# Kernel tuning notes

Measured on AMD Instinct MI355X. Metric: run time of the kernel, lower is better.

The kernel has to match this reference:

```python
import jax, jax.numpy as jnp
import numpy as np

N, G, D, H, F, L, NH_CI = 4096, 1024, 128, 4, 512, 2, 2
HD = D // H
LBD = 1.0
LS = 100.0  # length_scale, non-trainable


def setup_inputs() -> dict:
    key = jax.random.key(0)
    ks = jax.random.split(key, 40)
    s = 0.05
    r = lambda i, shape: (jax.random.normal(ks[i], shape, jnp.float32) * s)
    inp = {
        'raw_expr': jax.random.normal(ks[0], (N, G), jnp.float32),
        'sqr_pdist': jax.random.uniform(ks[1], (N, N), jnp.float32) * 1e4,
        'dn_W1': r(2, (G, 512)), 'dn_b1': jnp.zeros((512,), jnp.float32),
        'dn_W2': r(3, (512, G)), 'dn_b2': jnp.zeros((G,), jnp.float32),
        'q_W1': r(4, (G, 64)), 'q_b1': jnp.zeros((64,), jnp.float32),
        'q_W2': r(5, (64, 1)), 'q_b2': jnp.zeros((1,), jnp.float32),
        'e_Win': r(6, (G, D)), 'e_bin': jnp.zeros((D,), jnp.float32),
        'Wq': r(7, (L, D, D)), 'Wk': r(8, (L, D, D)),
        'Wv': r(9, (L, D, D)), 'Wo': r(10, (L, D, D)),
        'bq': jnp.zeros((L, D), jnp.float32), 'bk': jnp.zeros((L, D), jnp.float32),
        'bv': jnp.zeros((L, D), jnp.float32), 'bo': jnp.zeros((L, D), jnp.float32),
        'ln1_g': jnp.ones((L, D), jnp.float32), 'ln1_b': jnp.zeros((L, D), jnp.float32),
        'ln2_g': jnp.ones((L, D), jnp.float32), 'ln2_b': jnp.zeros((L, D), jnp.float32),
        'f_W1': r(11, (L, D, F)), 'f_b1': jnp.zeros((L, F), jnp.float32),
        'f_W2': r(12, (L, F, D)), 'f_b2': jnp.zeros((L, D), jnp.float32),
        'ci_T': r(13, (NH_CI, D, D)), 'ci_G': r(14, (NH_CI, G, G)),
        'interact': 1,
    }
    return inp


def _ln(x, g, b):
    m = jnp.mean(x, -1, keepdims=True)
    v = jnp.var(x, -1, keepdims=True)
    return g * (x - m) / jnp.sqrt(v + 1e-5) + b


def _forward(raw_expr, sqr_pdist, dn_W1, dn_b1, dn_W2, dn_b2,
             q_W1, q_b1, q_W2, q_b2, e_Win, e_bin,
             Wq, Wk, Wv, Wo, bq, bk, bv, bo,
             ln1_g, ln1_b, ln2_g, ln2_b, f_W1, f_b1, f_W2, f_b2,
             ci_T, ci_G, interact):
    n_cells = raw_expr.shape[0]
    # CellDenoise: residual MLP
    denoised = jax.nn.relu(raw_expr @ dn_W1 + dn_b1) @ dn_W2 + dn_b2 + raw_expr
    # CellQualify: [N, 1]
    quality = jnp.tanh(raw_expr @ q_W1 + q_b1) @ q_W2 + q_b2
    # CellEmbed: input proj + transformer encoder blocks over cells (no batch)
    h = raw_expr @ e_Win + e_bin  # [N, D]
    for l in range(L):
        q = (h @ Wq[l] + bq[l]).reshape(n_cells, H, HD)
        k = (h @ Wk[l] + bk[l]).reshape(n_cells, H, HD)
        v = (h @ Wv[l] + bv[l]).reshape(n_cells, H, HD)
        scores = jnp.einsum('nhd,mhd->hnm', q, k) / jnp.sqrt(jnp.float32(HD))
        attn = jax.nn.softmax(scores, axis=-1)
        o = jnp.einsum('hnm,mhd->nhd', attn, v).reshape(n_cells, D) @ Wo[l] + bo[l]
        h = _ln(h + o, ln1_g[l], ln1_b[l])
        ff = jax.nn.relu(h @ f_W1[l] + f_b1[l]) @ f_W2[l] + f_b2[l]
        h = _ln(h + ff, ln2_g[l], ln2_b[l])
    emb = h  # [N, D]
    # CellSmooth: softmax(-cdist + quality^T) @ denoised
    sq = jnp.sum(emb * emb, -1)
    d2 = jnp.maximum(sq[:, None] + sq[None, :] - 2.0 * emb @ emb.T, 0.0)
    dist = jnp.sqrt(d2)
    sim = jax.nn.softmax(-dist + quality.T, axis=-1)  # [N, N]
    smoothed = sim @ denoised  # [N, G]
    if interact:
        spatial = jnp.exp(-sqr_pdist / (LS * LS))  # [N, N]
        ci_out = jnp.zeros_like(smoothed)
        for hh in range(NH_CI):
            cell_inter = jax.nn.sigmoid(emb @ ci_T[hh] @ emb.T)  # [N, N]
            ci_out = ci_out + (spatial * cell_inter) @ smoothed @ ci_G[hh] / smoothed.shape[1]
        return smoothed + LBD * ci_out
    return smoothed


def reference(raw_expr, sqr_pdist, dn_W1, dn_b1, dn_W2, dn_b2,
              q_W1, q_b1, q_W2, q_b2, e_Win, e_bin,
              Wq, Wk, Wv, Wo, bq, bk, bv, bo,
              ln1_g, ln1_b, ln2_g, ln2_b, f_W1, f_b1, f_W2, f_b2,
              ci_T, ci_G, interact):
    return _forward(raw_expr, sqr_pdist, dn_W1, dn_b1, dn_W2, dn_b2,
                    q_W1, q_b1, q_W2, q_b2, e_Win, e_bin,
                    Wq, Wk, Wv, Wo, bq, bk, bv, bo,
                    ln1_g, ln1_b, ln2_g, ln2_b, f_W1, f_b1, f_W2, f_b2,
                    ci_T, ci_G, interact)
```

## Files before the change

### kernel.cpp

```cpp
#include <hip/hip_runtime.h>
#include <hip/hip_bf16.h>

#define NC 4096
#define GG 1024
#define DM 128
#define HH 4
#define HDIM 32
#define FF 512
#define LL 2
#define NHCI 2
#define NSF 16
#define LDV (NC+64)
#define LS2 (100.0f*100.0f)
#define QSCALE 0.17677669529663687f

typedef __bf16 bf16x8 __attribute__((ext_vector_type(8)));
typedef __bf16 bf16x4 __attribute__((ext_vector_type(4)));
typedef float  f32x4  __attribute__((ext_vector_type(4)));

__device__ __forceinline__ int xcd_swz(int orig, int nwg)
{
    int q = nwg >> 3, r = nwg & 7;
    int xcd = orig & 7, idx = orig >> 3;
    return (xcd < r ? xcd*(q+1) : r*(q+1) + (xcd-r)*q) + idx;
}

enum { MM_NONE=0, MM_BIAS, MM_BIAS_B16, MM_RELU_B16, MM_B16, MM_SIGSP_B16, MM_DIST };

template<int EM>
__launch_bounds__(256)
__global__ void mgemm_k(const __bf16* __restrict__ A, int lda,
                        const __bf16* __restrict__ BT, int ldb,
                        const float* __restrict__ aux1,
                        float* __restrict__ C, __bf16* __restrict__ Cb, int ldc,
                        int M, int N, int K, float alpha,
                        const float* __restrict__ aux2,
                        const int* __restrict__ flag)
{
    if (flag && *flag == 0) return;
    __shared__ __align__(16) __bf16 As[128][32];
    __shared__ __align__(16) __bf16 Bs[128][32];
    const int tid  = threadIdx.x;
    const int lane = tid & 63;
    const int wid  = tid >> 6;
    const int wm = wid >> 1, wn = wid & 1;
    const int nwg  = gridDim.x * gridDim.y;
    const int wg   = xcd_swz(blockIdx.y * gridDim.x + blockIdx.x, nwg);
    const int bm = (wg / gridDim.x) * 128, bn = (wg % gridDim.x) * 128;

    f32x4 acc[4][4];
    #pragma unroll
    for (int m=0;m<4;m++)
        #pragma unroll
        for (int n=0;n<4;n++) acc[m][n] = (f32x4){0.f,0.f,0.f,0.f};

    const int c0 = wid*64 + lane, c1 = c0 + 256;
    const __bf16* ga0 = A  + (size_t)(bm + (c0>>2))*lda + ((c0&3)<<3);
    const __bf16* ga1 = A  + (size_t)(bm + (c1>>2))*lda + ((c1&3)<<3);
    const __bf16* gb0 = BT + (size_t)(bn + (c0>>2))*ldb + ((c0&3)<<3);
    const __bf16* gb1 = BT + (size_t)(bn + (c1>>2))*ldb + ((c1&3)<<3);
    auto* lA = (__attribute__((address_space(3))) __bf16*)&As[0][0];
    auto* lB = (__attribute__((address_space(3))) __bf16*)&Bs[0][0];
    auto* lA0 = (__attribute__((address_space(3))) void*)(lA + (size_t)(wid*64)*8);
    auto* lA1 = (__attribute__((address_space(3))) void*)(lA + (size_t)(256 + wid*64)*8);
    auto* lB0 = (__attribute__((address_space(3))) void*)(lB + (size_t)(wid*64)*8);
    auto* lB1 = (__attribute__((address_space(3))) void*)(lB + (size_t)(256 + wid*64)*8);

    const int r  = lane & 15;
    const int kb = lane >> 4;
    const int arow = wm*64, brow = wn*64;

    for (int k0 = 0; k0 < K; k0 += 32) {
        __builtin_amdgcn_global_load_lds((const __attribute__((address_space(1))) void*)ga0, lA0, 16, 0, 0);
        __builtin_amdgcn_global_load_lds((const __attribute__((address_space(1))) void*)ga1, lA1, 16, 0, 0);
        __builtin_amdgcn_global_load_lds((const __attribute__((address_space(1))) void*)gb0, lB0, 16, 0, 0);
        __builtin_amdgcn_global_load_lds((const __attribute__((address_space(1))) void*)gb1, lB1, 16, 0, 0);
        ga0 += 32; ga1 += 32; gb0 += 32; gb1 += 32;
        __syncthreads();
        bf16x8 af[4], bfr[4];
        #pragma unroll
        for (int m=0;m<4;m++) af[m]  = *(const bf16x8*)&As[arow + m*16 + r][kb*8];
        #pragma unroll
        for (int n=0;n<4;n++) bfr[n] = *(const bf16x8*)&Bs[brow + n*16 + r][kb*8];
        #pragma unroll
        for (int m=0;m<4;m++)
            #pragma unroll
            for (int n=0;n<4;n++)
                acc[m][n] = __builtin_amdgcn_mfma_f32_16x16x32_bf16(af[m], bfr[n], acc[m][n], 0, 0, 0);
        __syncthreads();
    }

    const int crow = (lane >> 4) * 4;
    const int ccol = lane & 15;
    #pragma unroll
    for (int m=0;m<4;m++) {
        #pragma unroll
        for (int n=0;n<4;n++) {
            const int gn = bn + wn*64 + n*16 + ccol;
            #pragma unroll
            for (int q=0;q<4;q++) {
                const int gm = bm + wm*64 + m*16 + crow + q;
                float v = acc[m][n][q] * alpha;
                if (EM==MM_BIAS || EM==MM_BIAS_B16 || EM==MM_RELU_B16) v += aux1[gn];
                if (EM==MM_RELU_B16) v = fmaxf(v, 0.f);
                if (EM==MM_SIGSP_B16) {
                    v = 1.f/(1.f + __expf(-v));
                    v *= __expf(aux2[(size_t)(gm >> 1)*(size_t)N + gn] * (-1.f/LS2));
                }
                if (EM==MM_DIST) {
                    float d2 = fmaxf(aux2[gm] + aux2[gn] - 2.f*v, 0.f);
                    v = __expf(aux1[gn] - sqrtf(d2));
                }
                const size_t ci = (size_t)gm*ldc + gn;
                if (EM==MM_NONE || EM==MM_BIAS) C[ci] = v;
                else Cb[ci] = (__bf16)v;
            }
        }
    }
}

__launch_bounds__(256)
__global__ void mgemm_sk(const __bf16* __restrict__ A, int lda,
                         const __bf16* __restrict__ BT, int ldb,
                         __bf16* __restrict__ P, int M, int N, int KC,
                         const int* __restrict__ flag)
{
    if (flag && *flag == 0) return;
    __shared__ __align__(16) __bf16 As[128][32];
    __shared__ __align__(16) __bf16 Bs[128][32];
    const int tid  = threadIdx.x;
    const int lane = tid & 63;
    const int wid  = tid >> 6;
    const int wm = wid >> 1, wn = wid & 1;
    const int nwg  = gridDim.x * gridDim.y;
    const int wg   = xcd_swz(blockIdx.y * gridDim.x + blockIdx.x, nwg);
    const int bm = (wg / gridDim.x) * 128, bn = (wg % gridDim.x) * 128;
    const size_t koff = (size_t)blockIdx.z * KC;

    f32x4 acc[4][4];
    #pragma unroll
    for (int m=0;m<4;m++)
        #pragma unroll
        for (int n=0;n<4;n++) acc[m][n] = (f32x4){0.f,0.f,0.f,0.f};

    const int c0 = wid*64 + lane, c1 = c0 + 256;
    const __bf16* ga0 = A  + (size_t)(bm + (c0>>2))*lda + koff + ((c0&3)<<3);
    const __bf16* ga1 = A  + (size_t)(bm + (c1>>2))*lda + koff + ((c1&3)<<3);
    const __bf16* gb0 = BT + (size_t)(bn + (c0>>2))*ldb + koff + ((c0&3)<<3);
    const __bf16* gb1 = BT + (size_t)(bn + (c1>>2))*ldb + koff + ((c1&3)<<3);
    auto* lA = (__attribute__((address_space(3))) __bf16*)&As[0][0];
    auto* lB = (__attribute__((address_space(3))) __bf16*)&Bs[0][0];
    auto* lA0 = (__attribute__((address_space(3))) void*)(lA + (size_t)(wid*64)*8);
    auto* lA1 = (__attribute__((address_space(3))) void*)(lA + (size_t)(256 + wid*64)*8);
    auto* lB0 = (__attribute__((address_space(3))) void*)(lB + (size_t)(wid*64)*8);
    auto* lB1 = (__attribute__((address_space(3))) void*)(lB + (size_t)(256 + wid*64)*8);

    const int r  = lane & 15;
    const int kb = lane >> 4;
    const int arow = wm*64, brow = wn*64;

    for (int k0 = 0; k0 < KC; k0 += 32) {
        __builtin_amdgcn_global_load_lds((const __attribute__((address_space(1))) void*)ga0, lA0, 16, 0, 0);
        __builtin_amdgcn_global_load_lds((const __attribute__((address_space(1))) void*)ga1, lA1, 16, 0, 0);
        __builtin_amdgcn_global_load_lds((const __attribute__((address_space(1))) void*)gb0, lB0, 16, 0, 0);
        __builtin_amdgcn_global_load_lds((const __attribute__((address_space(1))) void*)gb1, lB1, 16, 0, 0);
        ga0 += 32; ga1 += 32; gb0 += 32; gb1 += 32;
        __syncthreads();
        bf16x8 af[4], bfr[4];
        #pragma unroll
        for (int m=0;m<4;m++) af[m]  = *(const bf16x8*)&As[arow + m*16 + r][kb*8];
        #pragma unroll
        for (int n=0;n<4;n++) bfr[n] = *(const bf16x8*)&Bs[brow + n*16 + r][kb*8];
        #pragma unroll
        for (int m=0;m<4;m++)
            #pragma unroll
            for (int n=0;n<4;n++)
                acc[m][n] = __builtin_amdgcn_mfma_f32_16x16x32_bf16(af[m], bfr[n], acc[m][n], 0, 0, 0);
        __syncthreads();
    }

    __bf16* Pz = P + (size_t)blockIdx.z * M * N;
    const int crow = (lane >> 4) * 4;
    const int ccol = lane & 15;
    #pragma unroll
    for (int m=0;m<4;m++)
        #pragma unroll
        for (int n=0;n<4;n++) {
            const int gn = bn + wn*64 + n*16 + ccol;
            #pragma unroll
            for (int q=0;q<4;q++) {
                const int gm = bm + wm*64 + m*16 + crow + q;
                Pz[(size_t)gm*N + gn] = (__bf16)acc[m][n][q];
            }
        }
}

enum { R_F32=0, R_B16LD, R_ACCG, R_RELU_B16, R_BRB16, R_TANH, R_BOTH, R_RS,
       R_BIAS16, R_BIASF, R_CIH, R_TEMB, R_QKVE };

template<int RE>
__launch_bounds__(256)
__global__ void redk_k(const __bf16* __restrict__ P, int M, int N, int KS,
                       const float* __restrict__ bias,
                       const float* __restrict__ res, int ldres,
                       float* __restrict__ C, __bf16* __restrict__ Cb,
                       int ldout, int coff,
                       const int* __restrict__ flag, float alpha)
{
    if (flag && *flag == 0) return;
    int i = blockIdx.x*256 + threadIdx.x;
    int total = (M*N) >> 2;
    if (i >= total) return;
    int row = i / (N >> 2);
    int c4  = (i - row*(N >> 2)) << 2;
    f32x4 s = {0.f,0.f,0.f,0.f};
    for (int ks = 0; ks < KS; ++ks) {
        bf16x4 t = *(const bf16x4*)(P + ((size_t)ks*M + row)*N + c4);
        s[0] += (float)t[0]; s[1] += (float)t[1];
        s[2] += (float)t[2]; s[3] += (float)t[3];
    }
    #pragma unroll
    for (int j=0;j<4;j++) {
        int col = c4 + j;
        float v = s[j];
        if (RE==R_RELU_B16) v = fmaxf(v + bias[col], 0.f);
        if (RE==R_BRB16)    v = v + bias[col] + res[(size_t)row*ldres + col];
        if (RE==R_TANH)     v = tanhf(v + bias[col]);
        if (RE==R_BOTH || RE==R_BIAS16 || RE==R_BIASF) v = v + bias[col];
        if (RE==R_QKVE)   { v = v + bias[col]; if (col < 128) v *= QSCALE; }
        if (RE==R_RS)       v = v * res[row];
        size_t o = (size_t)row*ldout + coff + col;
        if (RE==R_CIH)  o = (size_t)(row >> 1)*ldout + (size_t)(row & 1)*GG + col;
        if (RE==R_TEMB) o = ((size_t)row*2 + (col >> 7))*DM + (col & 127);
        if (RE==R_F32 || RE==R_TANH || RE==R_BIASF) C[o] = v;
        if (RE==R_BOTH) { C[o] = v; Cb[o] = (__bf16)v; }
        if (RE==R_RS)   { C[o] = v; Cb[o] = (__bf16)v; }
        if (RE==R_B16LD || RE==R_RELU_B16 || RE==R_BIAS16 || RE==R_CIH || RE==R_TEMB ||
            RE==R_QKVE || RE==R_BRB16) Cb[o] = (__bf16)v;
        if (RE==R_ACCG) C[o] += v * alpha;
    }
}

__launch_bounds__(64)
__global__ void redln_k(const __bf16* __restrict__ P, int KS,
                        const float* __restrict__ bias,
                        float* __restrict__ h, __bf16* __restrict__ hb,
                        const float* __restrict__ g, const float* __restrict__ b)
{
    int row = blockIdx.x, lane = threadIdx.x;
    float v0 = bias[lane], v1 = bias[lane + 64];
    for (int ks = 0; ks < KS; ++ks) {
        v0 += (float)P[((size_t)ks*NC + row)*DM + lane];
        v1 += (float)P[((size_t)ks*NC + row)*DM + lane + 64];
    }
    float x0 = h[row*DM + lane]      + v0;
    float x1 = h[row*DM + lane + 64] + v1;
    float s = x0 + x1, ss = x0*x0 + x1*x1;
    #pragma unroll
    for (int o=32;o>0;o>>=1) { s += __shfl_down(s, o); ss += __shfl_down(ss, o); }
    s = __shfl(s, 0); ss = __shfl(ss, 0);
    float mean = s * (1.f/128.f);
    float var  = ss * (1.f/128.f) - mean*mean;
    float inv  = rsqrtf(var + 1e-5f);
    float y0 = g[lane]      * (x0 - mean) * inv + b[lane];
    float y1 = g[lane + 64] * (x1 - mean) * inv + b[lane + 64];
    h[row*DM + lane]       = y0;  h[row*DM + lane + 64]  = y1;
    hb[row*DM + lane]      = (__bf16)y0;
    hb[row*DM + lane + 64] = (__bf16)y1;
}

__launch_bounds__(256)
__global__ void flashp_k(const __bf16* __restrict__ Q, const __bf16* __restrict__ Kb,
                         int ldqk, const __bf16* __restrict__ VT, int ldv,
                         __bf16* __restrict__ Op, float* __restrict__ lp)
{
    __shared__ __align__(16) __bf16 Plds[4][64][68];
    const int lane = threadIdx.x & 63, w = threadIdx.x >> 6;
    const int hd = blockIdx.y, sp = blockIdx.z;
    const int q0 = blockIdx.x * 256 + w * 64;
    const int c  = lane & 15, kb = lane >> 4;

    bf16x8 aq[4];
    #pragma unroll
    for (int qs=0;qs<4;qs++)
        aq[qs] = *(const bf16x8*)&Q[(size_t)(q0 + qs*16 + c)*ldqk + hd*HDIM + kb*8];
    bf16x8 ones;
    #pragma unroll
    for (int j=0;j<8;j++) ones[j] = (__bf16)1.0f;

    f32x4 oacc[4][2];
    f32x4 lacc[4];
    #pragma unroll
    for (int qs=0;qs<4;qs++) {
        oacc[qs][0] = (f32x4){0,0,0,0}; oacc[qs][1] = (f32x4){0,0,0,0};
        lacc[qs] = (f32x4){0,0,0,0};
    }

    const int kv0 = sp * (NC/NSF), kv1 = kv0 + NC/NSF;
    for (int kv = kv0; kv < kv1; kv += 64) {
        bf16x8 bk[4];
        #pragma unroll
        for (int n=0;n<4;n++)
            bk[n] = *(const bf16x8*)&Kb[(size_t)(kv + n*16 + c)*ldqk + hd*HDIM + kb*8];
        bf16x8 bv[2][2];
        #pragma unroll
        for (int ks=0;ks<2;ks++)
            #pragma unroll
            for (int n2=0;n2<2;n2++)
                bv[ks][n2] = *(const bf16x8*)&VT[(size_t)(hd*HDIM + n2*16 + c)*ldv + kv + ks*32 + kb*8];
        #pragma unroll
        for (int qs=0;qs<4;qs++) {
            f32x4 s[4];
            #pragma unroll
            for (int n=0;n<4;n++)
                s[n] = __builtin_amdgcn_mfma_f32_16x16x32_bf16(aq[qs], bk[n], (f32x4){0,0,0,0}, 0, 0, 0);
            #pragma unroll
            for (int n=0;n<4;n++)
                #pragma unroll
                for (int q=0;q<4;q++)
                    Plds[w][qs*16 + kb*4 + q][n*16 + c] = (__bf16)__expf(s[n][q]);
        }
        #pragma unroll
        for (int qs=0;qs<4;qs++)
            #pragma unroll
            for (int ks=0;ks<2;ks++) {
                bf16x8 ap = *(const bf16x8*)&Plds[w][qs*16 + c][ks*32 + kb*8];
                #pragma unroll
                for (int n2=0;n2<2;n2++)
                    oacc[qs][n2] = __builtin_amdgcn_mfma_f32_16x16x32_bf16(ap, bv[ks][n2], oacc[qs][n2], 0, 0, 0);
                lacc[qs] = __builtin_amdgcn_mfma_f32_16x16x32_bf16(ap, ones, lacc[qs], 0, 0, 0);
            }
    }
    __bf16* Oz = Op + (size_t)sp * NC * DM;
    #pragma unroll
    for (int qs=0;qs<4;qs++)
        #pragma unroll
        for (int n2=0;n2<2;n2++)
            #pragma unroll
            for (int q=0;q<4;q++)
                Oz[(size_t)(q0 + qs*16 + kb*4 + q)*DM + hd*HDIM + n2*16 + c] = (__bf16)oacc[qs][n2][q];
    if (c == 0) {
        #pragma unroll
        for (int qs=0;qs<4;qs++)
            #pragma unroll
            for (int q=0;q<4;q++)
                lp[((size_t)sp*HH + hd)*NC + q0 + qs*16 + kb*4 + q] = lacc[qs][q];
    }
}

__launch_bounds__(256)
__global__ void flashmerge_k(const __bf16* __restrict__ Op, const float* __restrict__ lp,
                             __bf16* __restrict__ O)
{
    int idx = blockIdx.x*256 + threadIdx.x;
    int row = idx >> 7, col = idx & 127, hd = col >> 5;
    float L = 0.f, acc = 0.f;
    #pragma unroll
    for (int s=0;s<NSF;s++) {
        L   += lp[((size_t)s*HH + hd)*NC + row];
        acc += (float)Op[(size_t)s*NC*DM + idx];
    }
    O[idx] = (__bf16)(acc / L);
}

__device__ __forceinline__ void tconv32(float (*tile)[33],
                                        const float* __restrict__ in,
                                        __bf16* __restrict__ out,
                                        int R, int C, int ldout, int coff, int t)
{
    int tx = threadIdx.x & 31, ty = threadIdx.x >> 5;
    int bx = t % (C/32), by = t / (C/32);
    int bc = bx*32, br = by*32;
    #pragma unroll
    for (int i=0;i<4;i++)
        tile[ty + 8*i][tx] = in[(size_t)(br + ty + 8*i)*C + bc + tx];
    __syncthreads();
    #pragma unroll
    for (int i=0;i<4;i++)
        out[(size_t)(bc + ty + 8*i)*ldout + coff + br + tx] = (__bf16)tile[tx][ty + 8*i];
}

__launch_bounds__(256)
__global__ void megaprep_k(const float* __restrict__ dn_W1, const float* __restrict__ dn_W2,
                           const float* __restrict__ e_Win, const float* __restrict__ q_W1,
                           const float* __restrict__ q_b1,
                           const float* __restrict__ Wq, const float* __restrict__ Wk,
                           const float* __restrict__ Wv,
                           const float* __restrict__ bq, const float* __restrict__ bk,
                           const float* __restrict__ bv,
                           const float* __restrict__ Wo, const float* __restrict__ f_W1,
                           const float* __restrict__ f_W2,
                           const float* __restrict__ ci_T, const float* __restrict__ ci_G,
                           const float* __restrict__ raw,
                           __bf16* __restrict__ dnW1T, __bf16* __restrict__ dnW2T,
                           __bf16* __restrict__ eWinT, __bf16* __restrict__ qW1pT,
                           float* __restrict__ qb1p,
                           __bf16* __restrict__ Wqkv, float* __restrict__ bqkv,
                           __bf16* __restrict__ WoT, __bf16* __restrict__ fW1T,
                           __bf16* __restrict__ fW2T, __bf16* __restrict__ ciTT,
                           __bf16* __restrict__ ciGbigT, __bf16* __restrict__ rawB,
                           const int* __restrict__ interact)
{
    __shared__ float tile[32][33];
    int t = blockIdx.x;
    if (t < 512) { tconv32(tile, dn_W1, dnW1T, GG, FF, GG, 0, t); return; }
    t -= 512;
    if (t < 512) { tconv32(tile, dn_W2, dnW2T, FF, GG, FF, 0, t); return; }
    t -= 512;
    if (t < 128) { tconv32(tile, e_Win, eWinT, GG, DM, GG, 0, t); return; }
    t -= 128;
    if (t < 512) {
        int idx = t*256 + threadIdx.x;
        int k = idx & 1023, j = idx >> 10;
        qW1pT[(size_t)j*GG + k] = (j < 64) ? (__bf16)q_W1[(size_t)k*64 + j] : (__bf16)0.f;
        return;
    }
    t -= 512;
    if (t < 1) {
        if (threadIdx.x < 128) qb1p[threadIdx.x] = (threadIdx.x < 64) ? q_b1[threadIdx.x] : 0.f;
        return;
    }
    t -= 1;
    if (t < 384) {
        int l = t / 192;
        int i = (t % 192)*256 + threadIdx.x;
        int n = i >> 7, k = i & 127;
        const float* W = (n < 128) ? Wq : (n < 256 ? Wk : Wv);
        Wqkv[(size_t)l*384*128 + i] = (__bf16)W[(size_t)l*DM*DM + (size_t)k*DM + (n & 127)];
        if (i < 384) {
            const float* b = (i < 128) ? bq : (i < 256 ? bk : bv);
            bqkv[l*384 + i] = b[l*DM + (i & 127)];
        }
        return;
    }
    t -= 384;
    if (t < 32) { int l = t/16; tconv32(tile, Wo + (size_t)l*DM*DM, WoT + (size_t)l*DM*DM, DM, DM, DM, 0, t%16); return; }
    t -= 32;
    if (t < 128) { int l = t/64; tconv32(tile, f_W1 + (size_t)l*DM*FF, fW1T + (size_t)l*FF*DM, DM, FF, DM, 0, t%64); return; }
    t -= 128;
    if (t < 128) { int l = t/64; tconv32(tile, f_W2 + (size_t)l*FF*DM, fW2T + (size_t)l*DM*FF, FF, DM, FF, 0, t%64); return; }
    t -= 128;
    if (t < 32) {
        if (*interact) { int l = t/16; tconv32(tile, ci_T + (size_t)l*DM*DM, ciTT + (size_t)l*DM*DM, DM, DM, DM, 0, t%16); }
        return;
    }
    t -= 32;
    if (t < 2048) {
        if (*interact) { int hh = t/1024; tconv32(tile, ci_G + (size_t)hh*GG*GG, ciGbigT, GG, GG, 2*GG, hh*GG, t%1024); }
        return;
    }
    t -= 2048;
    {
        int i = t*256 + threadIdx.x;
        float4 v = ((const float4*)raw)[i];
        bf16x4 o = {(__bf16)v.x, (__bf16)v.y, (__bf16)v.z, (__bf16)v.w};
        ((bf16x4*)rawB)[i] = o;
    }
}

__global__ void qualify2_k(const float* __restrict__ Tq, const float* __restrict__ w,
                           const float* __restrict__ b2, float* __restrict__ quality)
{
    int row = blockIdx.x, lane = threadIdx.x;
    float v = Tq[row*128 + lane] * w[lane];
    #pragma unroll
    for (int o=32;o>0;o>>=1) v += __shfl_down(v, o);
    if (lane == 0) quality[row] = v + b2[0];
}

__global__ void rownorm_k(const float* __restrict__ h, float* __restrict__ sq)
{
    int row = blockIdx.x, lane = threadIdx.x;
    float x0 = h[row*DM + lane], x1 = h[row*DM + lane + 64];
    float v = x0*x0 + x1*x1;
    #pragma unroll
    for (int o=32;o>0;o>>=1) v += __shfl_down(v, o);
    if (lane == 0) sq[row] = v;
}

__launch_bounds__(256)
__global__ void rowsum16_k(const __bf16* __restrict__ P, float* __restrict__ rinv)
{
    __shared__ float sl[4];
    size_t row = blockIdx.x;
    const __bf16* p = P + row * (size_t)NC;
    int tid = threadIdx.x;
    float sum = 0.f;
    for (int j = tid*8; j < NC; j += 256*8) {
        bf16x8 v = *(const bf16x8*)&p[j];
        #pragma unroll
        for (int k=0;k<8;k++) sum += (float)v[k];
    }
    #pragma unroll
    for (int o=32;o>0;o>>=1) sum += __shfl_down(sum, o);
    if ((tid & 63) == 0) sl[tid >> 6] = sum;
    __syncthreads();
    if (tid == 0) rinv[row] = 1.f / (sl[0] + sl[1] + sl[2] + sl[3]);
}

__global__ void tconv16_k(const __bf16* __restrict__ in, int ldin, int coff,
                          __bf16* __restrict__ out, int ldout)
{
    __shared__ __bf16 tile[32][33];
    int bc = blockIdx.x * 32, br = blockIdx.y * 32;
    int tx = threadIdx.x & 31, ty = threadIdx.x >> 5;
    #pragma unroll
    for (int i=0;i<4;i++)
        tile[ty + 8*i][tx] = in[(size_t)(br + ty + 8*i)*ldin + coff + bc + tx];
    __syncthreads();
    #pragma unroll
    for (int i=0;i<4;i++)
        out[(size_t)(bc + ty + 8*i)*ldout + br + tx] = tile[tx][ty + 8*i];
}

static void mg(int em, const __bf16* A, int lda, const __bf16* BT, int ldb,
               const float* aux1, float* C, __bf16* Cb, int ldc,
               int M, int N, int K, float alpha,
               const float* aux2, const int* flag, hipStream_t s)
{
    dim3 grid(N/128, M/128), block(256);
#define MGL(E) mgemm_k<E><<<grid,block,0,s>>>(A,lda,BT,ldb,aux1,C,Cb,ldc,M,N,K,alpha,aux2,flag)
    switch (em) {
        case MM_NONE:      MGL(MM_NONE);      break;
        case MM_BIAS:      MGL(MM_BIAS);      break;
        case MM_BIAS_B16:  MGL(MM_BIAS_B16);  break;
        case MM_RELU_B16:  MGL(MM_RELU_B16);  break;
        case MM_B16:       MGL(MM_B16);       break;
        case MM_SIGSP_B16: MGL(MM_SIGSP_B16); break;
        case MM_DIST:      MGL(MM_DIST);      break;
    }
#undef MGL
}

static void sk(const __bf16* A, int lda, const __bf16* BT, int ldb,
               __bf16* P, int M, int N, int K, int KS, const int* flag, hipStream_t s)
{
    dim3 grid(N/128, M/128, KS), block(256);
    mgemm_sk<<<grid, block, 0, s>>>(A, lda, BT, ldb, P, M, N, K/KS, flag);
}

static void red(int re, const __bf16* P, int M, int N, int KS,
                const float* bias, const float* res, int ldres,
                float* C, __bf16* Cb, int ldout, int coff,
                const int* flag, float alpha, hipStream_t s)
{
    int blocks = (M*N/4 + 255) / 256;
#define RDL(E) redk_k<E><<<blocks,256,0,s>>>(P,M,N,KS,bias,res,ldres,C,Cb,ldout,coff,flag,alpha)
    switch (re) {
        case R_F32:      RDL(R_F32);      break;
        case R_B16LD:    RDL(R_B16LD);    break;
        case R_ACCG:     RDL(R_ACCG);     break;
        case R_RELU_B16: RDL(R_RELU_B16); break;
        case R_BRB16:    RDL(R_BRB16);    break;
        case R_TANH:     RDL(R_TANH);     break;
        case R_BOTH:     RDL(R_BOTH);     break;
        case R_RS:       RDL(R_RS);       break;
        case R_BIAS16:   RDL(R_BIAS16);   break;
        case R_BIASF:    RDL(R_BIASF);    break;
        case R_CIH:      RDL(R_CIH);      break;
        case R_TEMB:     RDL(R_TEMB);     break;
        case R_QKVE:     RDL(R_QKVE);     break;
    }
#undef RDL
}

extern "C" void kernel_launch(void* const* d_in, const int* in_sizes, int n_in,
                              void* d_out, int out_size, void* d_ws, size_t ws_size,
                              hipStream_t stream)
{
    const float* raw   = (const float*)d_in[0];
    const float* spd   = (const float*)d_in[1];
    const float* dn_W1 = (const float*)d_in[2];
    const float* dn_b1 = (const float*)d_in[3];
    const float* dn_W2 = (const float*)d_in[4];
    const float* dn_b2 = (const float*)d_in[5];
    const float* q_W1  = (const float*)d_in[6];
    const float* q_b1  = (const float*)d_in[7];
    const float* q_W2  = (const float*)d_in[8];
    const float* q_b2  = (const float*)d_in[9];
    const float* e_Win = (const float*)d_in[10];
    const float* e_bin = (const float*)d_in[11];
    const float* Wq    = (const float*)d_in[12];
    const float* Wk    = (const float*)d_in[13];
    const float* Wv    = (const float*)d_in[14];
    const float* Wo    = (const float*)d_in[15];
    const float* bq    = (const float*)d_in[16];
    const float* bk    = (const float*)d_in[17];
    const float* bv    = (const float*)d_in[18];
    const float* bo    = (const float*)d_in[19];
    const float* ln1_g = (const float*)d_in[20];
    const float* ln1_b = (const float*)d_in[21];
    const float* ln2_g = (const float*)d_in[22];
    const float* ln2_b = (const float*)d_in[23];
    const float* f_W1  = (const float*)d_in[24];
    const float* f_b1  = (const float*)d_in[25];
    const float* f_W2  = (const float*)d_in[26];
    const float* f_b2  = (const float*)d_in[27];
    const float* ci_T  = (const float*)d_in[28];
    const float* ci_G  = (const float*)d_in[29];
    const int*   interact = (const int*)d_in[30];
    (void)in_sizes; (void)n_in; (void)ws_size; (void)out_size;

    float* out = (float*)d_out;
    float* ws = (float*)d_ws;
    size_t off = 0;
    auto af32 = [&](size_t n) { float* p = ws + off; off += n; return p; };
    auto ab16 = [&](size_t n) { __bf16* p = (__bf16*)(ws + off); off += (n + 1) / 2; return p; };

    float*  S        = af32((size_t)NC * NC);
    __bf16* simB     = ab16((size_t)NC * NC);
    __bf16* ciS2     = ab16((size_t)NC * NC);
    __bf16* denB     = ab16((size_t)NC * GG);
    __bf16* smoB     = ab16((size_t)NC * GG);
    __bf16* T1b      = ab16((size_t)NC * FF);
    float*  Tq       = af32((size_t)NC * 128);
    float*  quality  = af32(NC);
    float*  rowinv   = af32(NC);
    float*  h        = af32((size_t)NC * DM);
    __bf16* hb       = ab16((size_t)NC * DM);
    __bf16* qkvB     = ab16((size_t)NC * 384);
    __bf16* vbT      = ab16((size_t)DM * LDV);
    __bf16* obB      = ab16((size_t)NC * DM);
    __bf16* rawB     = ab16((size_t)NC * GG);
    __bf16* denT     = ab16((size_t)GG * NC);
    __bf16* smoT     = ab16((size_t)GG * NC);
    __bf16* Ubig     = ab16((size_t)NC * 2*GG);
    __bf16* TembBig  = ab16((size_t)NHCI * NC * DM);
    float*  sqbuf    = af32(NC);
    __bf16* dnW1T    = ab16((size_t)FF * GG);
    __bf16* dnW2T    = ab16((size_t)GG * FF);
    __bf16* eWinT    = ab16((size_t)DM * GG);
    __bf16* qW1pT    = ab16((size_t)128 * GG);
    float*  qb1p     = af32(128);
    __bf16* Wqkv     = ab16((size_t)LL * 384 * DM);
    float*  bqkv     = af32((size_t)LL * 384);
    __bf16* WoT      = ab16((size_t)LL * DM * DM);
    __bf16* fW1T     = ab16((size_t)LL * FF * DM);
    __bf16* fW2T     = ab16((size_t)LL * DM * FF);
    __bf16* ciTT     = ab16((size_t)NHCI * DM * DM);
    __bf16* ciGbigT  = ab16((size_t)GG * 2*GG);
    (void)ciS2;

    __bf16* Pb      = (__bf16*)S;
    __bf16* Opart   = (__bf16*)S;
    float*  lpart   = (float*)(Opart + (size_t)NSF*NC*DM);
    __bf16* ciSbig  = simB;

    megaprep_k<<<8513, 256, 0, stream>>>(dn_W1, dn_W2, e_Win, q_W1, q_b1,
                                         Wq, Wk, Wv, bq, bk, bv,
                                         Wo, f_W1, f_W2, ci_T, ci_G, raw,
                                         dnW1T, dnW2T, eWinT, qW1pT, qb1p,
                                         Wqkv, bqkv, WoT, fW1T, fW2T,
                                         ciTT, ciGbigT, rawB, interact);

    sk(rawB, GG, dnW1T, GG, Pb, NC, FF, GG, 8, nullptr, stream);
    red(R_RELU_B16, Pb, NC, FF, 8, dn_b1, nullptr, 0, nullptr, T1b, FF, 0, nullptr, 1.f, stream);
    sk(T1b, FF, dnW2T, FF, Pb, NC, GG, FF, 4, nullptr, stream);
    red(R_BRB16, Pb, NC, GG, 4, dn_b2, raw, GG, nullptr, denB, GG, 0, nullptr, 1.f, stream);
    sk(rawB, GG, qW1pT, GG, Pb, NC, 128, GG, 8, nullptr, stream);
    red(R_TANH, Pb, NC, 128, 8, qb1p, nullptr, 0, Tq, nullptr, 128, 0, nullptr, 1.f, stream);
    qualify2_k<<<NC, 64, 0, stream>>>(Tq, q_W2, q_b2, quality);
    sk(rawB, GG, eWinT, GG, Pb, NC, 128, GG, 8, nullptr, stream);
    red(R_BOTH, Pb, NC, 128, 8, e_bin, nullptr, 0, h, hb, 128, 0, nullptr, 1.f, stream);
    for (int l = 0; l < LL; ++l) {
        sk(hb, DM, Wqkv + (size_t)l*384*DM, DM, Pb, NC, 384, DM, 2, nullptr, stream);
        red(R_QKVE, Pb, NC, 384, 2, bqkv + l*384, nullptr, 0, nullptr, qkvB, 384, 0,
            nullptr, 1.f, stream);
        tconv16_k<<<dim3(DM/32, NC/32), 256, 0, stream>>>(qkvB, 384, 256, vbT, LDV);
        flashp_k<<<dim3(NC/256, HH, NSF), 256, 0, stream>>>(qkvB, qkvB + 128, 384, vbT, LDV,
                                                            Opart, lpart);
        flashmerge_k<<<(NC*DM)/256, 256, 0, stream>>>(Opart, lpart, obB);
        sk(obB, DM, WoT + (size_t)l*DM*DM, DM, Pb, NC, DM, DM, 4, nullptr, stream);
        redln_k<<<NC, 64, 0, stream>>>(Pb, 4, bo + l*DM, h, hb, ln1_g + l*DM, ln1_b + l*DM);
        sk(hb, DM, fW1T + (size_t)l*FF*DM, DM, Pb, NC, FF, DM, 2, nullptr, stream);
        red(R_RELU_B16, Pb, NC, FF, 2, f_b1 + l*FF, nullptr, 0, nullptr, T1b, FF, 0,
            nullptr, 1.f, stream);
        sk(T1b, FF, fW2T + (size_t)l*DM*FF, FF, Pb, NC, DM, FF, 4, nullptr, stream);
        redln_k<<<NC, 64, 0, stream>>>(Pb, 4, f_b2 + l*DM, h, hb, ln2_g + l*DM, ln2_b + l*DM);
    }
    rownorm_k<<<NC, 64, 0, stream>>>(h, sqbuf);
    mg(MM_DIST, hb, DM, hb, DM, quality, nullptr, simB, NC, NC, NC, DM, 1.f,
       sqbuf, nullptr, stream);
    rowsum16_k<<<NC, 256, 0, stream>>>(simB, rowinv);
    tconv16_k<<<dim3(GG/32, NC/32), 256, 0, stream>>>(denB, GG, 0, denT, NC);
    sk(simB, NC, denT, NC, Pb, NC, GG, NC, 4, nullptr, stream);
    red(R_RS, Pb, NC, GG, 4, nullptr, rowinv, 0, out, smoB, GG, 0, nullptr, 1.f, stream);
    tconv16_k<<<dim3(GG/32, NC/32), 256, 0, stream>>>(smoB, GG, 0, smoT, NC);
    sk(hb, DM, ciTT, DM, Pb, NC, 256, DM, 4, interact, stream);
    red(R_TEMB, Pb, NC, 256, 4, nullptr, nullptr, 0, nullptr, TembBig, 0, 0,
        interact, 1.f, stream);
    mg(MM_SIGSP_B16, TembBig, DM, hb, DM, nullptr,
       nullptr, ciSbig, NC, 2*NC, NC, DM, 1.f, spd, interact, stream);
    sk(ciSbig, NC, smoT, NC, Pb, 2*NC, GG, NC, 4, interact, stream);
    red(R_CIH, Pb, 2*NC, GG, 4, nullptr, nullptr, 0, nullptr, Ubig, 2*GG, 0,
        interact, 1.f, stream);
    sk(Ubig, 2*GG, ciGbigT, 2*GG, Pb, NC, GG, 2*GG, 4, interact, stream);
    red(R_ACCG, Pb, NC, GG, 4, nullptr, nullptr, 0, out, nullptr, GG, 0,
        interact, 1.0f/1024.f, stream);
}
```

Before: 589.6 us.

## Add 256x256-tile split-K GEMM with LDS-pipelined loads for large GEMMs

Adds a new 512-thread GEMM kernel with 256x256 output tiles. It loads directly into 128KB of LDS through global_load_lds, uses a multi-stage software pipeline with explicit vmcnt waits, and raises wave priority around the MFMA blocks. The three largest K=4096/2048 GEMMs (sim@denoised, cell-interaction@smoothed, U@ciG) switch to it, and split-K for the interaction GEMM drops from 4 to 2. The larger tiles are meant to cut global/L2 traffic per FLOP and hide load latency. The cost is one workgroup per CU, fewer workgroups overall, and a fragile hand-tuned wait schedule.

```diff
diff --git a/kernel.cpp b/kernel.cpp
--- a/kernel.cpp
+++ b/kernel.cpp
@@ -190,6 +190,149 @@
             #pragma unroll
             for (int q=0;q<4;q++) {
                 const int gm = bm + wm*64 + m*16 + crow + q;
+                Pz[(size_t)gm*N + gn] = (__bf16)acc[m][n][q];
+            }
+        }
+}
+
+__launch_bounds__(512, 1)
+__global__ void mg256_sk(const __bf16* __restrict__ A, int lda,
+                         const __bf16* __restrict__ BT, int ldb,
+                         __bf16* __restrict__ P, int M, int N, int KC,
+                         const int* __restrict__ flag)
+{
+    if (flag && *flag == 0) return;
+    extern __shared__ __align__(16) __bf16 lds[];
+    auto* L3 = (__attribute__((address_space(3))) __bf16*)lds;
+    const int tid  = threadIdx.x;
+    const int lane = tid & 63, w = tid >> 6;
+    const int wm = w >> 2, wn = w & 3;
+    const int nwg = gridDim.x * gridDim.y;
+    const int wg  = xcd_swz(blockIdx.y * gridDim.x + blockIdx.x, nwg);
+    const int bm = (wg / gridDim.x) * 256, bn = (wg % gridDim.x) * 256;
+    const size_t koff = (size_t)blockIdx.z * KC;
+    const int NT = KC / 64;
+    const int r = lane & 15, kb = lane >> 4;
+
+    f32x4 acc[8][4];
+    #pragma unroll
+    for (int m=0;m<8;m++)
+        #pragma unroll
+        for (int n=0;n<4;n++) acc[m][n] = (f32x4){0.f,0.f,0.f,0.f};
+
+    auto stage = [&](const __bf16* src, int ld, int brc, int kt, int s, int region) {
+        #pragma unroll
+        for (int j = 0; j < 2; ++j) {
+            int c = j*512 + tid;
+            const __bf16* g = src + (size_t)(brc + (c>>2))*ld + koff + (size_t)kt*64 + s*32 + ((c&3)<<3);
+            __builtin_amdgcn_global_load_lds(
+                (const __attribute__((address_space(1))) void*)g,
+                (__attribute__((address_space(3))) void*)(L3 + region + (j*512 + w*64)*8),
+                16, 0, 0);
+        }
+    };
+    auto ldsA = [&](int d, int s, int m) -> bf16x8 {
+        return *(const bf16x8*)&lds[(d*2+s)*8192 + (wm*128 + m*16 + r)*32 + kb*8];
+    };
+    auto ldsB = [&](int d, int s, int n) -> bf16x8 {
+        return *(const bf16x8*)&lds[32768 + (d*2+s)*8192 + (wn*64 + n*16 + r)*32 + kb*8];
+    };
+
+    stage(A,  lda, bm, 0, 0, 0*8192);
+    stage(BT, ldb, bn, 0, 0, 32768 + 0*8192);
+    stage(A,  lda, bm, 0, 1, 1*8192);
+    stage(BT, ldb, bn, 0, 1, 32768 + 1*8192);
+    stage(A,  lda, bm, 1, 0, 2*8192);
+    stage(BT, ldb, bn, 1, 0, 32768 + 2*8192);
+    asm volatile("s_waitcnt vmcnt(8)" ::: "memory");
+    __builtin_amdgcn_s_barrier();
+
+    for (int i = 0; i < NT/2; ++i) {
+        const int t1 = 2*i+1, t2 = 2*i+2, t3 = 2*i+3;
+        bf16x8 bf[4], af[4];
+
+#define MG256_MFMA(MB) \
+        __builtin_amdgcn_s_barrier(); \
+        __builtin_amdgcn_s_setprio(1); \
+        _Pragma("unroll") \
+        for (int mi=0; mi<4; ++mi) \
+            _Pragma("unroll") \
+            for (int n=0; n<4; ++n) \
+                acc[MB+mi][n] = __builtin_amdgcn_mfma_f32_16x16x32_bf16(af[mi], bf[n], acc[MB+mi][n], 0, 0, 0); \
+        __builtin_amdgcn_s_setprio(0);
+
+        #pragma unroll
+        for (int n=0;n<4;n++)  bf[n] = ldsB(0,0,n);
+        #pragma unroll
+        for (int mi=0;mi<4;mi++) af[mi] = ldsA(0,0,mi);
+        stage(A, lda, bm, t1, 1, 3*8192);
+        MG256_MFMA(0)
+        __builtin_amdgcn_s_barrier();
+        #pragma unroll
+        for (int mi=0;mi<4;mi++) af[mi] = ldsA(0,0,4+mi);
+        stage(BT, ldb, bn, t1, 1, 32768 + 3*8192);
+        MG256_MFMA(4)
+        asm volatile("s_waitcnt vmcnt(8)" ::: "memory");
+        __builtin_amdgcn_s_barrier();
+
+        #pragma unroll
+        for (int n=0;n<4;n++)  bf[n] = ldsB(0,1,n);
+        #pragma unroll
+        for (int mi=0;mi<4;mi++) af[mi] = ldsA(0,1,mi);
+        if (t2 < NT) stage(A, lda, bm, t2, 0, 0*8192);
+        MG256_MFMA(0)
+        __builtin_amdgcn_s_barrier();
+        #pragma unroll
+        for (int mi=0;mi<4;mi++) af[mi] = ldsA(0,1,4+mi);
+        if (t2 < NT) stage(BT, ldb, bn, t2, 0, 32768 + 0*8192);
+        MG256_MFMA(4)
+        if (t2 < NT) { asm volatile("s_waitcnt vmcnt(8)" ::: "memory"); }
+        else         { asm volatile("s_waitcnt vmcnt(4)" ::: "memory"); }
+        __builtin_amdgcn_s_barrier();
+
+        #pragma unroll
+        for (int n=0;n<4;n++)  bf[n] = ldsB(1,0,n);
+        #pragma unroll
+        for (int mi=0;mi<4;mi++) af[mi] = ldsA(1,0,mi);
+        if (t2 < NT) stage(A, lda, bm, t2, 1, 1*8192);
+        MG256_MFMA(0)
+        __builtin_amdgcn_s_barrier();
+        #pragma unroll
+        for (int mi=0;mi<4;mi++) af[mi] = ldsA(1,0,4+mi);
+        if (t2 < NT) stage(BT, ldb, bn, t2, 1, 32768 + 1*8192);
+        MG256_MFMA(4)
+        if (t2 < NT) { asm volatile("s_waitcnt vmcnt(8)" ::: "memory"); }
+        else         { asm volatile("s_waitcnt vmcnt(0)" ::: "memory"); }
+        __builtin_amdgcn_s_barrier();
+
+        #pragma unroll
+        for (int n=0;n<4;n++)  bf[n] = ldsB(1,1,n);
+        #pragma unroll
+        for (int mi=0;mi<4;mi++) af[mi] = ldsA(1,1,mi);
+        if (t3 < NT) stage(A, lda, bm, t3, 0, 2*8192);
+        MG256_MFMA(0)
+        __builtin_amdgcn_s_barrier();
+        #pragma unroll
+        for (int mi=0;mi<4;mi++) af[mi] = ldsA(1,1,4+mi);
+        if (t3 < NT) stage(BT, ldb, bn, t3, 0, 32768 + 2*8192);
+        MG256_MFMA(4)
+        if (t3 < NT) { asm volatile("s_waitcnt vmcnt(8)" ::: "memory"); }
+        __builtin_amdgcn_s_barrier();
+#undef MG256_MFMA
+    }
+    asm volatile("s_waitcnt vmcnt(0)" ::: "memory");
+
+    __bf16* Pz = P + (size_t)blockIdx.z * M * N;
+    const int crow = (lane >> 4) * 4;
+    const int ccol = lane & 15;
+    #pragma unroll
+    for (int m=0;m<8;m++)
+        #pragma unroll
+        for (int n=0;n<4;n++) {
+            const int gn = bn + wn*64 + n*16 + ccol;
+            #pragma unroll
+            for (int q=0;q<4;q++) {
+                const int gm = bm + wm*128 + m*16 + crow + q;
                 Pz[(size_t)gm*N + gn] = (__bf16)acc[m][n][q];
             }
         }
@@ -537,6 +680,13 @@
 {
     dim3 grid(N/128, M/128, KS), block(256);
     mgemm_sk<<<grid, block, 0, s>>>(A, lda, BT, ldb, P, M, N, K/KS, flag);
+}
+
+static void sk256(const __bf16* A, int lda, const __bf16* BT, int ldb,
+                  __bf16* P, int M, int N, int K, int KS, const int* flag, hipStream_t s)
+{
+    dim3 grid(N/256, M/256, KS), block(512);
+    mg256_sk<<<grid, block, 131072, s>>>(A, lda, BT, ldb, P, M, N, K/KS, flag);
 }
 
 static void red(int re, const __bf16* P, int M, int N, int KS,
@@ -600,6 +750,9 @@
     const float* ci_G  = (const float*)d_in[29];
     const int*   interact = (const int*)d_in[30];
     (void)in_sizes; (void)n_in; (void)ws_size; (void)out_size;
+
+    (void)hipFuncSetAttribute((const void*)mg256_sk,
+                              hipFuncAttributeMaxDynamicSharedMemorySize, 131072);
 
     float* out = (float*)d_out;
     float* ws = (float*)d_ws;
@@ -683,7 +836,7 @@
        sqbuf, nullptr, stream);
     rowsum16_k<<<NC, 256, 0, stream>>>(simB, rowinv);
     tconv16_k<<<dim3(GG/32, NC/32), 256, 0, stream>>>(denB, GG, 0, denT, NC);
-    sk(simB, NC, denT, NC, Pb, NC, GG, NC, 4, nullptr, stream);
+    sk256(simB, NC, denT, NC, Pb, NC, GG, NC, 4, nullptr, stream);
     red(R_RS, Pb, NC, GG, 4, nullptr, rowinv, 0, out, smoB, GG, 0, nullptr, 1.f, stream);
     tconv16_k<<<dim3(GG/32, NC/32), 256, 0, stream>>>(smoB, GG, 0, smoT, NC);
     sk(hb, DM, ciTT, DM, Pb, NC, 256, DM, 4, interact, stream);
@@ -691,10 +844,10 @@
         interact, 1.f, stream);
     mg(MM_SIGSP_B16, TembBig, DM, hb, DM, nullptr,
        nullptr, ciSbig, NC, 2*NC, NC, DM, 1.f, spd, interact, stream);
-    sk(ciSbig, NC, smoT, NC, Pb, 2*NC, GG, NC, 4, interact, stream);
-    red(R_CIH, Pb, 2*NC, GG, 4, nullptr, nullptr, 0, nullptr, Ubig, 2*GG, 0,
+    sk256(ciSbig, NC, smoT, NC, Pb, 2*NC, GG, NC, 2, interact, stream);
+    red(R_CIH, Pb, 2*NC, GG, 2, nullptr, nullptr, 0, nullptr, Ubig, 2*GG, 0,
         interact, 1.f, stream);
-    sk(Ubig, 2*GG, ciGbigT, 2*GG, Pb, NC, GG, 2*GG, 4, interact, stream);
+    sk256(Ubig, 2*GG, ciGbigT, 2*GG, Pb, NC, GG, 2*GG, 4, interact, stream);
     red(R_ACCG, Pb, NC, GG, 4, nullptr, nullptr, 0, out, nullptr, GG, 0,
         interact, 1.0f/1024.f, stream);
 }
```

After: 522.1 us. 1.13x faster.
